# Performance work log

Measured on AMD Instinct MI355X. Metric: run time of the kernel, lower is better.

The kernel has to match this reference:

```python
import jax, jax.numpy as jnp
import numpy as np

VOCAB = 32000
DIM = 256
LAYERS = 2
CLASSES = 8
BATCH = 32
SEQ = 8192


def setup_inputs() -> dict:
    key = jax.random.key(0)
    ks = jax.random.split(key, 8)
    s = 1.0 / np.sqrt(DIM)
    x = jax.random.randint(ks[0], (BATCH, SEQ), 0, VOCAB, dtype=jnp.int32)
    emb = jax.random.normal(ks[1], (VOCAB, DIM), dtype=jnp.float32)
    Wz = jax.random.normal(ks[2], (LAYERS, DIM, DIM), dtype=jnp.float32) * s
    bz = jnp.zeros((LAYERS, DIM), dtype=jnp.float32)
    Wh = jax.random.normal(ks[3], (LAYERS, DIM, DIM), dtype=jnp.float32) * s
    bh = jnp.zeros((LAYERS, DIM), dtype=jnp.float32)
    Wo = jax.random.normal(ks[4], (DIM, CLASSES), dtype=jnp.float32) * s
    bo = jnp.zeros((CLASSES,), dtype=jnp.float32)
    return {"x": x, "emb": emb, "Wz": Wz, "bz": bz, "Wh": Wh, "bh": bh, "Wo": Wo, "bo": bo}


def _min_gru_layer(h_in, Wz_l, bz_l, Wh_l, bh_l):
    # minGRU: z_t = sigmoid(W_z x_t); h~_t = W_h x_t
    # h_t = (1 - z_t) * h_{t-1} + z_t * h~_t,  h_0 = 0
    z = jax.nn.sigmoid(jnp.einsum('bsd,de->bse', h_in, Wz_l) + bz_l)
    h_tilde = jnp.einsum('bsd,de->bse', h_in, Wh_l) + bh_l
    a = 1.0 - z          # decay coefficient
    b = z * h_tilde      # input contribution
    # parallel associative scan of h_t = a_t * h_{t-1} + b_t (h_0 = 0)
    def combine(c1, c2):
        a1, b1 = c1
        a2, b2 = c2
        return a1 * a2, b1 * a2 + b2
    _, h = jax.lax.associative_scan(combine, (a, b), axis=1)
    return h


def reference(x, emb, Wz, bz, Wh, bh, Wo, bo):
    h = emb[x]  # [B, S, D]
    for l in range(LAYERS):
        h = _min_gru_layer(h, Wz[l], bz[l], Wh[l], bh[l])
    # classifier on the last timestep
    return h[:, -1] @ Wo + bo  # [B, CLASSES]
```

## Files before the change

kernel.cpp:

```cpp
#include <hip/hip_runtime.h>
#include <stdint.h>

#define SEQ 8192
#define CS 64
#define NCH 128
#define HB2 16
#define HBLK (HB2 * NCH)

typedef float f32x4 __attribute__((ext_vector_type(4)));
typedef short short8 __attribute__((ext_vector_type(8)));
typedef unsigned short u16;
typedef u16 ushort8 __attribute__((ext_vector_type(8)));
typedef u16 ushort4v __attribute__((ext_vector_type(4)));

__device__ __forceinline__ u16 f2bf(float f) {
  uint32_t u = __float_as_uint(f);
  u += 0x7fffu + ((u >> 16) & 1u);
  return (u16)(u >> 16);
}
__device__ __forceinline__ float bf2f(uint32_t lo16) {
  return __uint_as_float(lo16 << 16);
}

__device__ __forceinline__ void gld16(void* lds, const void* g) {
  __builtin_amdgcn_global_load_lds(
      (const __attribute__((address_space(1))) uint32_t*)g,
      (__attribute__((address_space(3))) uint32_t*)lds, 16, 0, 0);
}

__global__ void embq_kernel(const float* __restrict__ emb, u16* __restrict__ embq) {
  int i = (blockIdx.x * 256 + threadIdx.x) * 4;
  float4 v = *(const float4*)(emb + i);
  ushort4v p;
  p[0] = f2bf(v.x); p[1] = f2bf(v.y); p[2] = f2bf(v.z); p[3] = f2bf(v.w);
  *(ushort4v*)(embq + i) = p;
}

__global__ void wt_kernel(const float* __restrict__ Wz, const float* __restrict__ Wh,
                          u16* __restrict__ WtS) {
  int idx = blockIdx.x * 256 + threadIdx.x;
  int d = idx & 255;
  int k = (idx >> 8) & 255;
  int m = idx >> 16;
  const float* src = (m < 2 ? Wz : Wh) + (size_t)(m & 1) * 65536;
  float v = src[k * 256 + d];
  int dh = d >> 6, dloc = d & 63, k32 = k >> 5, kl = k & 31;
  size_t tile = ((size_t)(m * 4 + dh) * 8 + k32) * 4096;
  size_t byte = (size_t)(dloc * 64 + ((kl * 2) ^ (((dloc >> 1) & 3) << 4)));
  *(u16*)((char*)WtS + tile + byte) = f2bf(v);
}

__device__ __forceinline__ void stage32(char* dst_wave, const char* WtSb, int mat, int k32,
                                        int w, int lane) {
  const char* src = WtSb + ((size_t)((mat * 4 + w) * 8 + k32)) * 4096 + lane * 16;
  #pragma unroll
  for (int i = 0; i < 4; i++)
    gld16(dst_wave + i * 1024, src + i * 1024);
}

__device__ __forceinline__ void load_fa(const u16* As, int k32, int l15, int lg,
                                        short8 (&fa)[4]) {
  const int xm = (l15 & 7) << 4;
  const int kt = k32 >> 1, ks = k32 & 1;
  #pragma unroll
  for (int mi = 0; mi < 4; mi++)
    fa[mi] = *(const short8*)((const char*)As + kt * 8192 +
               (((mi * 16 + l15) * 128 + ks * 64 + lg * 16) ^ xm));
}

__device__ __forceinline__ void mfma_frags(const char* Pw, const short8 (&fa)[4],
    int l15, int lg, f32x4 (&acc)[4][4])
{
  #pragma unroll
  for (int ni = 0; ni < 4; ni++) {
    const int dloc = ni * 16 + l15;
    const int off = dloc * 64 + ((lg * 16) ^ (((dloc >> 1) & 3) << 4));
    short8 fb = *(const short8*)(Pw + off);
    #pragma unroll
    for (int mi = 0; mi < 4; mi++)
      acc[mi][ni] = __builtin_amdgcn_mfma_f32_16x16x32_bf16(fa[mi], fb, acc[mi][ni], 0, 0, 0);
  }
}

__device__ __forceinline__ void gemm_pipe3(int lsel, const char* WtSb, const u16* As,
    char* Pw, int w, int l15, int lg, int lane,
    f32x4 (&accz)[4][4], f32x4 (&acch)[4][4])
{
  stage32(Pw,         WtSb, lsel,     0, w, lane);
  stage32(Pw + 16384, WtSb, 2 + lsel, 0, w, lane);
  short8 fa[4];
  #pragma unroll
  for (int i = 0; i < 16; ++i) {
    if (i < 15) asm volatile("s_waitcnt vmcnt(4)" ::: "memory");
    else        asm volatile("s_waitcnt vmcnt(0)" ::: "memory");
    __builtin_amdgcn_sched_barrier(0);
    if (i + 2 < 16)
      stage32(Pw + ((i + 2) % 3) * 16384, WtSb,
              ((i + 2) & 1) ? (2 + lsel) : lsel, (i + 2) >> 1, w, lane);
    if ((i & 1) == 0) {
      load_fa(As, i >> 1, l15, lg, fa);
      mfma_frags(Pw + (i % 3) * 16384, fa, l15, lg, accz);
    } else {
      mfma_frags(Pw + (i % 3) * 16384, fa, l15, lg, acch);
    }
  }
}

__device__ __forceinline__ float2* seg_ptr(char* segt, int s, int d) {
  return (float2*)(segt + s * 2048 + ((d * 8) ^ (s << 4)));
}

template<int PHASE>
__global__ __launch_bounds__(256, 2)
void gru_kernel(const int* __restrict__ x, const u16* __restrict__ embq,
                const u16* __restrict__ WtS,
                const float* __restrict__ bz0, const float* __restrict__ bh0,
                const float* __restrict__ bz1, const float* __restrict__ bh1,
                const float* __restrict__ carry, uint32_t* __restrict__ ab,
                float* __restrict__ Ap, float* __restrict__ Bs)
{
  __shared__ __align__(16) u16 As[16384];
  __shared__ __align__(16) char Pb[49152];

  const int tid = threadIdx.x;
  const int lane = tid & 63;
  const int w = tid >> 6;
  const int l15 = lane & 15, lg = lane >> 4;
  const int cb = blockIdx.x;
  const int b = cb >> 7, c = cb & (NCH - 1);
  const char* WtSb = (const char*)WtS;
  char* segt = (char*)As;
  char* Pw = Pb + w * 4096;

  f32x4 accz[4][4], acch[4][4];
  #pragma unroll
  for (int i = 0; i < 4; i++)
    #pragma unroll
    for (int j = 0; j < 4; j++) {
      f32x4 zz = {0.f, 0.f, 0.f, 0.f};
      accz[i][j] = zz; acch[i][j] = zz;
    }

  if (PHASE == 0) {
    {
      const int sm = tid >> 2, kq = tid & 3;
      const int tok = x[b * SEQ + c * CS + sm];
      const u16* src = embq + (size_t)tok * 256 + kq * 64;
      char* sub = (char*)As + kq * 8192;
      const int swz = (sm & 7) << 4;
      #pragma unroll
      for (int j = 0; j < 8; j++) {
        ushort8 p = *(const ushort8*)(src + j * 8);
        *(ushort8*)(sub + ((sm * 128 + j * 16) ^ swz)) = p;
      }
    }
    __syncthreads();
    gemm_pipe3(0, WtSb, As, Pw, w, l15, lg, lane, accz, acch);
    __syncthreads();

    #pragma unroll
    for (int ni = 0; ni < 4; ni++) {
      const int d = w * 64 + ni * 16 + l15;
      const float bzv = bz0[d];
      const float bhv = bh0[d];
      #pragma unroll
      for (int mi = 0; mi < 4; mi++) {
        float A = 1.f, B = 0.f;
        #pragma unroll
        for (int r = 0; r < 4; r++) {
          float zl = accz[mi][ni][r] + bzv;
          float a = __builtin_amdgcn_rcpf(1.f + __expf(zl));
          float ht = acch[mi][ni][r] + bhv;
          float bb = (1.f - a) * ht;
          const int t = mi * 16 + lg * 4 + r;
          ab[(size_t)cb * 16384 + t * 256 + d] =
              (uint32_t)f2bf(a) | ((uint32_t)f2bf(bb) << 16);
          B = B * a + bb;
          A *= a;
        }
        *seg_ptr(segt, mi * 4 + lg, d) = make_float2(A, B);
      }
    }
    __syncthreads();
    {
      float PA = 1.f, PB = 0.f;
      #pragma unroll
      for (int s = 0; s < 16; s++) {
        float2 v = *seg_ptr(segt, s, tid);
        PB = v.x * PB + v.y;
        PA *= v.x;
      }
      Ap[(size_t)cb * 256 + tid] = PA;
      Bs[(size_t)cb * 256 + tid] = PB;
    }
    return;
  }

  {
    const int d = tid;
    float h = carry[(size_t)cb * 256 + d];
    const uint32_t* pab = ab + (size_t)cb * 16384 + d;
    char* sub = (char*)As + (d >> 6) * 8192;
    const int kl2 = (d & 63) * 2;
    #pragma unroll 8
    for (int t = 0; t < CS; t++) {
      uint32_t u = pab[(size_t)t * 256];
      h = bf2f(u & 0xffffu) * h + bf2f(u >> 16);
      *(u16*)(sub + ((t * 128 + kl2) ^ ((t & 7) << 4))) = f2bf(h);
    }
  }
  __syncthreads();
  gemm_pipe3(1, WtSb, As, Pw, w, l15, lg, lane, accz, acch);
  __syncthreads();

  #pragma unroll
  for (int ni = 0; ni < 4; ni++) {
    const int d = w * 64 + ni * 16 + l15;
    const float bzv = bz1[d];
    const float bhv = bh1[d];
    #pragma unroll
    for (int mi = 0; mi < 4; mi++) {
      float A = 1.f, B = 0.f;
      #pragma unroll
      for (int r = 0; r < 4; r++) {
        float zl = accz[mi][ni][r] + bzv;
        float a = __builtin_amdgcn_rcpf(1.f + __expf(zl));
        float ht = acch[mi][ni][r] + bhv;
        float bb = (1.f - a) * ht;
        B = B * a + bb;
        A *= a;
      }
      *seg_ptr(segt, mi * 4 + lg, d) = make_float2(A, B);
    }
  }
  __syncthreads();
  {
    float PA = 1.f, PB = 0.f;
    #pragma unroll
    for (int s = 0; s < 16; s++) {
      float2 v = *seg_ptr(segt, s, tid);
      PB = v.x * PB + v.y;
      PA *= v.x;
    }
    Ap[(size_t)cb * 256 + tid] = PA;
    Bs[(size_t)cb * 256 + tid] = PB;
  }
}

__global__ void scan2_l0(const float* __restrict__ Ap0, const float* __restrict__ Bs0,
                         float* __restrict__ carry) {
  const int g = blockIdx.x * 256 + threadIdx.x;
  const int b = g >> 8, d = g & 255;
  float h = 0.f;
  for (int c = 0; c < NCH; c++) {
    const size_t idx = (size_t)(b * NCH + c) * 256 + d;
    carry[idx] = h;
    h = Bs0[idx] + Ap0[idx] * h;
  }
}

__global__ void scan2_l1(const float* __restrict__ Ap1, const float* __restrict__ Bs1,
                         float* __restrict__ hlast) {
  const int g = blockIdx.x * 256 + threadIdx.x;
  const int b = g >> 8, d = g & 255;
  float h = 0.f;
  for (int c = 0; c < NCH; c++) {
    const size_t idx = (size_t)(b * NCH + c) * 256 + d;
    h = Bs1[idx] + Ap1[idx] * h;
  }
  hlast[b * 256 + d] = h;
}

__global__ void cls_kernel(const float* __restrict__ hlast, const float* __restrict__ Wo,
                           const float* __restrict__ bo, float* __restrict__ out) {
  const int t = threadIdx.x;
  const int b = t >> 3, c = t & 7;
  float acc = bo[c];
  for (int d = 0; d < 256; d++) acc += hlast[b * 256 + d] * Wo[d * 8 + c];
  out[t] = acc;
}

extern "C" void kernel_launch(void* const* d_in, const int* in_sizes, int n_in,
                              void* d_out, int out_size, void* d_ws, size_t ws_size,
                              hipStream_t stream) {
  (void)in_sizes; (void)n_in; (void)out_size; (void)ws_size;
  const int*   x   = (const int*)d_in[0];
  const float* emb = (const float*)d_in[1];
  const float* Wz  = (const float*)d_in[2];
  const float* bz  = (const float*)d_in[3];
  const float* Wh  = (const float*)d_in[4];
  const float* bh  = (const float*)d_in[5];
  const float* Wo  = (const float*)d_in[6];
  const float* bo  = (const float*)d_in[7];
  float* out = (float*)d_out;
  char* ws = (char*)d_ws;

  u16*      embq  = (u16*)     (ws);
  u16*      WtS   = (u16*)     (ws + 16777216ull);
  float*    Ap0   = (float*)   (ws + 17301504ull);
  float*    Bs0   = (float*)   (ws + 19398656ull);
  float*    carry = (float*)   (ws + 21495808ull);
  float*    Ap1   = (float*)   (ws + 23592960ull);
  float*    Bs1   = (float*)   (ws + 27787264ull);
  float*    hlast = (float*)   (ws + 31981568ull);
  uint32_t* ab    = (uint32_t*)(ws + 32014336ull);

  embq_kernel<<<8000, 256, 0, stream>>>(emb, embq);
  wt_kernel<<<1024, 256, 0, stream>>>(Wz, Wh, WtS);

  for (int hf = 0; hf < 2; hf++) {
    const int* xh = x + (size_t)hf * HB2 * SEQ;
    gru_kernel<0><<<HBLK, 256, 0, stream>>>(
        xh, embq, WtS, bz, bh, bz + 256, bh + 256, nullptr, ab, Ap0, Bs0);
    scan2_l0<<<HB2, 256, 0, stream>>>(Ap0, Bs0, carry);
    gru_kernel<1><<<HBLK, 256, 0, stream>>>(
        xh, embq, WtS, bz, bh, bz + 256, bh + 256, carry, ab,
        Ap1 + (size_t)hf * HBLK * 256, Bs1 + (size_t)hf * HBLK * 256);
  }

  scan2_l1<<<32, 256, 0, stream>>>(Ap1, Bs1, hlast);
  cls_kernel<<<1, 256, 0, stream>>>(hlast, Wo, bo, out);
}
```

Measured before the change: 271.3 us.

## Load weight fragments directly into registers and relayout ab buffer for coalesced stores

Replaces the LDS-staged triple-buffered weight pipeline (global_load_lds into a 48KB shared buffer) with direct per-lane global loads of B fragments into registers, double-buffered across k-steps. This removes the large LDS allocation, which may allow more blocks per CU, and removes the waitcnt/barrier choreography. The intermediate ab buffer layout is also permuted so phase-0 stores follow the MFMA output order and are contiguous, with the phase-1 reader index updated to match and fully unrolled. The cost is more VGPRs for the prefetched fragments and reliance on the cache for weight reuse across waves.

```diff
diff --git a/kernel.cpp b/kernel.cpp
--- a/kernel.cpp
+++ b/kernel.cpp
@@ -20,12 +20,6 @@
 }
 __device__ __forceinline__ float bf2f(uint32_t lo16) {
   return __uint_as_float(lo16 << 16);
-}
-
-__device__ __forceinline__ void gld16(void* lds, const void* g) {
-  __builtin_amdgcn_global_load_lds(
-      (const __attribute__((address_space(1))) uint32_t*)g,
-      (__attribute__((address_space(3))) uint32_t*)lds, 16, 0, 0);
 }
 
 __global__ void embq_kernel(const float* __restrict__ emb, u16* __restrict__ embq) {
@@ -50,14 +44,6 @@
   *(u16*)((char*)WtS + tile + byte) = f2bf(v);
 }
 
-__device__ __forceinline__ void stage32(char* dst_wave, const char* WtSb, int mat, int k32,
-                                        int w, int lane) {
-  const char* src = WtSb + ((size_t)((mat * 4 + w) * 8 + k32)) * 4096 + lane * 16;
-  #pragma unroll
-  for (int i = 0; i < 4; i++)
-    gld16(dst_wave + i * 1024, src + i * 1024);
-}
-
 __device__ __forceinline__ void load_fa(const u16* As, int k32, int l15, int lg,
                                         short8 (&fa)[4]) {
   const int xm = (l15 & 7) << 4;
@@ -68,40 +54,48 @@
                (((mi * 16 + l15) * 128 + ks * 64 + lg * 16) ^ xm));
 }
 
-__device__ __forceinline__ void mfma_frags(const char* Pw, const short8 (&fa)[4],
-    int l15, int lg, f32x4 (&acc)[4][4])
+__device__ __forceinline__ void gemm_pipe_reg(int lsel, const char* WtSb, const u16* As,
+    int w, int l15, int lg, f32x4 (&accz)[4][4], f32x4 (&acch)[4][4])
 {
+  const char* bz = WtSb + ((size_t)((lsel * 4 + w) * 8)) * 4096;
+  const char* bh = WtSb + ((size_t)(((2 + lsel) * 4 + w) * 8)) * 4096;
+  int offs[4];
   #pragma unroll
   for (int ni = 0; ni < 4; ni++) {
     const int dloc = ni * 16 + l15;
-    const int off = dloc * 64 + ((lg * 16) ^ (((dloc >> 1) & 3) << 4));
-    short8 fb = *(const short8*)(Pw + off);
-    #pragma unroll
-    for (int mi = 0; mi < 4; mi++)
-      acc[mi][ni] = __builtin_amdgcn_mfma_f32_16x16x32_bf16(fa[mi], fb, acc[mi][ni], 0, 0, 0);
-  }
-}
-
-__device__ __forceinline__ void gemm_pipe3(int lsel, const char* WtSb, const u16* As,
-    char* Pw, int w, int l15, int lg, int lane,
-    f32x4 (&accz)[4][4], f32x4 (&acch)[4][4])
-{
-  stage32(Pw,         WtSb, lsel,     0, w, lane);
-  stage32(Pw + 16384, WtSb, 2 + lsel, 0, w, lane);
+    offs[ni] = dloc * 64 + ((lg * 16) ^ (((dloc >> 1) & 3) << 4));
+  }
+  short8 pz[4], ph[4];
+  #pragma unroll
+  for (int ni = 0; ni < 4; ni++) {
+    pz[ni] = *(const short8*)(bz + offs[ni]);
+    ph[ni] = *(const short8*)(bh + offs[ni]);
+  }
   short8 fa[4];
   #pragma unroll
-  for (int i = 0; i < 16; ++i) {
-    if (i < 15) asm volatile("s_waitcnt vmcnt(4)" ::: "memory");
-    else        asm volatile("s_waitcnt vmcnt(0)" ::: "memory");
-    __builtin_amdgcn_sched_barrier(0);
-    if (i + 2 < 16)
-      stage32(Pw + ((i + 2) % 3) * 16384, WtSb,
-              ((i + 2) & 1) ? (2 + lsel) : lsel, (i + 2) >> 1, w, lane);
-    if ((i & 1) == 0) {
-      load_fa(As, i >> 1, l15, lg, fa);
-      mfma_frags(Pw + (i % 3) * 16384, fa, l15, lg, accz);
-    } else {
-      mfma_frags(Pw + (i % 3) * 16384, fa, l15, lg, acch);
+  for (int k32 = 0; k32 < 8; k32++) {
+    short8 nz[4], nh[4];
+    if (k32 < 7) {
+      #pragma unroll
+      for (int ni = 0; ni < 4; ni++) {
+        nz[ni] = *(const short8*)(bz + (k32 + 1) * 4096 + offs[ni]);
+        nh[ni] = *(const short8*)(bh + (k32 + 1) * 4096 + offs[ni]);
+      }
+    }
+    load_fa(As, k32, l15, lg, fa);
+    #pragma unroll
+    for (int ni = 0; ni < 4; ni++)
+      #pragma unroll
+      for (int mi = 0; mi < 4; mi++)
+        accz[mi][ni] = __builtin_amdgcn_mfma_f32_16x16x32_bf16(fa[mi], pz[ni], accz[mi][ni], 0, 0, 0);
+    #pragma unroll
+    for (int ni = 0; ni < 4; ni++)
+      #pragma unroll
+      for (int mi = 0; mi < 4; mi++)
+        acch[mi][ni] = __builtin_amdgcn_mfma_f32_16x16x32_bf16(fa[mi], ph[ni], acch[mi][ni], 0, 0, 0);
+    if (k32 < 7) {
+      #pragma unroll
+      for (int ni = 0; ni < 4; ni++) { pz[ni] = nz[ni]; ph[ni] = nh[ni]; }
     }
   }
 }
@@ -109,6 +103,7 @@
 __device__ __forceinline__ float2* seg_ptr(char* segt, int s, int d) {
   return (float2*)(segt + s * 2048 + ((d * 8) ^ (s << 4)));
 }
+
 
 template<int PHASE>
 __global__ __launch_bounds__(256, 2)
@@ -120,7 +115,6 @@
                 float* __restrict__ Ap, float* __restrict__ Bs)
 {
   __shared__ __align__(16) u16 As[16384];
-  __shared__ __align__(16) char Pb[49152];
 
   const int tid = threadIdx.x;
   const int lane = tid & 63;
@@ -130,7 +124,6 @@
   const int b = cb >> 7, c = cb & (NCH - 1);
   const char* WtSb = (const char*)WtS;
   char* segt = (char*)As;
-  char* Pw = Pb + w * 4096;
 
   f32x4 accz[4][4], acch[4][4];
   #pragma unroll
@@ -155,7 +148,7 @@
       }
     }
     __syncthreads();
-    gemm_pipe3(0, WtSb, As, Pw, w, l15, lg, lane, accz, acch);
+    gemm_pipe_reg(0, WtSb, As, w, l15, lg, accz, acch);
     __syncthreads();
 
     #pragma unroll
@@ -172,8 +165,7 @@
           float a = __builtin_amdgcn_rcpf(1.f + __expf(zl));
           float ht = acch[mi][ni][r] + bhv;
           float bb = (1.f - a) * ht;
-          const int t = mi * 16 + lg * 4 + r;
-          ab[(size_t)cb * 16384 + t * 256 + d] =
+          ab[(size_t)cb * 16384 + (size_t)((mi * 64 + r * 16 + ni * 4 + w) * 64 + lg * 16 + l15)] =
               (uint32_t)f2bf(a) | ((uint32_t)f2bf(bb) << 16);
           B = B * a + bb;
           A *= a;
@@ -199,18 +191,19 @@
   {
     const int d = tid;
     float h = carry[(size_t)cb * 256 + d];
-    const uint32_t* pab = ab + (size_t)cb * 16384 + d;
+    const uint32_t* pab = ab + (size_t)cb * 16384 +
+                          (size_t)((((d >> 4) & 3) * 4 + (d >> 6)) * 64 + (d & 15));
     char* sub = (char*)As + (d >> 6) * 8192;
     const int kl2 = (d & 63) * 2;
-    #pragma unroll 8
+    #pragma unroll
     for (int t = 0; t < CS; t++) {
-      uint32_t u = pab[(size_t)t * 256];
+      uint32_t u = pab[(t >> 4) * 4096 + (t & 3) * 1024 + ((t >> 2) & 3) * 16];
       h = bf2f(u & 0xffffu) * h + bf2f(u >> 16);
       *(u16*)(sub + ((t * 128 + kl2) ^ ((t & 7) << 4))) = f2bf(h);
     }
   }
   __syncthreads();
-  gemm_pipe3(1, WtSb, As, Pw, w, l15, lg, lane, accz, acch);
+  gemm_pipe_reg(1, WtSb, As, w, l15, lg, accz, acch);
   __syncthreads();
 
   #pragma unroll
```

Result: slower. 310.3 us (+14.4%).
